# Optimization experiments

Hardware: AMD Instinct MI355X
Metric: run time of the kernel (lower is better)

Reference implementation:

```python
import jax, jax.numpy as jnp
import numpy as np

ACTION_NS = [3, 3, 2, 4, 24]        # forward_back, left_right, jump, sneak_sprint, attack_...
RANGE_STARTS = [6, 8, 10, 11, 14]   # action_ranges starts (indices 0..5 are commit + camera ops)
N_ACTIONS = 37
LOGIT_DIM = 36
MIN_DELTA = 0.5 / 2**3
MAX_STEP = 20
MAX_CAMSTEP = 6
B, NUM_INPUT, HIDDEN = 32768, 1024, 2048
D_IN = NUM_INPUT + 4 + LOGIT_DIM


def setup_inputs():
    key = jax.random.key(0)
    ks = jax.random.split(key, 12)
    inp = {
        "fc_input": jax.random.normal(ks[0], (B, NUM_INPUT), jnp.float32),
        "camera": jax.random.normal(ks[1], (B, 2), jnp.float32),
        "rand_u": jax.random.uniform(ks[2], (B,), jnp.float32),
        "W1": (jax.random.normal(ks[3], (D_IN, HIDDEN), jnp.float32) / np.sqrt(D_IN)).astype(jnp.float32),
        "b1": jnp.zeros((HIDDEN,), jnp.float32),
        "W2": (jax.random.normal(ks[4], (HIDDEN, N_ACTIONS), jnp.float32) / np.sqrt(HIDDEN)).astype(jnp.float32),
        "b2": jnp.zeros((N_ACTIONS,), jnp.float32),
    }
    names = ["act_fb", "act_lr", "act_jp", "act_ss", "act_atk"]
    for i, (nm, n) in enumerate(zip(names, ACTION_NS)):
        inp[nm] = jax.random.randint(ks[5 + i], (B,), 0, n, jnp.int32)
    return inp


def _discretize_scan(camera, acts):
    # Faithful jax version of the 20-step no_grad target/input construction loop.
    nB = camera.shape[0]
    cam0, cam1 = camera[:, 0], camera[:, 1]

    def step(carry, _):
        ac, delta, rdac, dch, cam_steps, committed, norm = carry
        oh = [jax.nn.one_hot(r, n, dtype=jnp.float32) for r, n in zip(rdac, ACTION_NS)]
        inp_vec = jnp.concatenate([ac] + oh + [delta[:, None], dch.astype(jnp.float32)[:, None]], axis=1)  # [B,40]
        norm = norm + (~committed).astype(jnp.float32)
        commit = ((jnp.abs(cam0) < 1e-5) & (jnp.abs(cam1) < 1e-5)) | (cam_steps >= MAX_CAMSTEP)
        for r, a in zip(rdac, acts):
            commit = commit & (r == a)
        dac = jnp.zeros((nB,), jnp.int32)
        modified = commit
        new_rdac = []
        for r, a, rs in zip(rdac, acts, RANGE_STARTS):
            disc = (~modified) & (r != a)
            dac = jnp.where(disc & (a == 0), r - 1 + rs, jnp.where(disc, a - 1 + rs, dac))
            new_rdac.append(jnp.where(disc, a, r))
            modified = modified | disc
        d2 = delta * 2.0
        # NOTE: original torch code compares cam[:,1] against ac[:,0]; bug preserved.
        dmask = (~modified) & (~dch) & ((jnp.abs(cam0 - ac[:, 0]) > d2) | (jnp.abs(cam1 - ac[:, 0]) > d2))
        dac = jnp.where(dmask, 5, dac)
        delta = jnp.where(dmask, jnp.clip(d2, -0.5, 0.5), delta)
        modified = modified | dmask
        sx = jnp.where(cam0 < ac[:, 0], -1.0, 1.0)
        sy = jnp.where(cam1 < ac[:, 1], -1.0, 1.0)
        quad = jnp.where(sx < 0, jnp.where(sy < 0, 1, 3), jnp.where(sy < 0, 2, 4)).astype(jnp.int32)
        dac = jnp.where(~modified, quad, dac)
        move = jnp.stack([sx, sy], axis=1) * delta[:, None]
        ac = jnp.where((~modified)[:, None], ac + move, ac)
        delta = jnp.where(~modified, delta * 0.5, delta)
        dch = dch | (~modified)
        cam_steps = cam_steps + (~modified).astype(jnp.int32)
        committed = committed | commit
        return (ac, delta, tuple(new_rdac), dch, cam_steps, committed, norm), (inp_vec, dac)

    init = (jnp.zeros((nB, 2), jnp.float32),
            jnp.full((nB,), MIN_DELTA, jnp.float32),
            tuple(jnp.zeros((nB,), jnp.int32) for _ in ACTION_NS),
            jnp.zeros((nB,), bool),
            jnp.zeros((nB,), jnp.int32),
            jnp.zeros((nB,), bool),
            jnp.zeros((nB,), jnp.float32))
    carry, (all_inputs, all_dacs) = jax.lax.scan(step, init, None, length=MAX_STEP)
    return all_inputs, all_dacs, carry[-1]  # [T,B,40], [T,B], norm [B]


def reference(fc_input, camera, rand_u, W1, b1, W2, b2, act_fb, act_lr, act_jp, act_ss, act_atk):
    acts = (act_fb, act_lr, act_jp, act_ss, act_atk)
    all_inputs, all_dacs, norm = _discretize_scan(camera, acts)
    rand_sam = jnp.minimum((rand_u * norm).astype(jnp.int32), MAX_STEP - 1)  # sample an uncommitted step
    idx = jnp.arange(fc_input.shape[0])
    sel = jax.lax.stop_gradient(all_inputs[rand_sam, idx])  # [B,40]
    tgt = jax.lax.stop_gradient(all_dacs[rand_sam, idx])    # [B]
    x = jnp.concatenate([fc_input, sel], axis=1)
    h = x @ W1 + b1
    h = h * jax.nn.sigmoid(h)  # swish
    logits = h @ W2 + b2
    logp = jax.nn.log_softmax(logits, axis=-1)
    loss = -jnp.take_along_axis(logp, tgt[:, None], axis=1)[:, 0]  # per-sample CE (reduction='none')
    return loss
```

## Files before the change

kernel.cpp:

```cpp
#include <hip/hip_runtime.h>
#include <hip/hip_bf16.h>
#include <stdint.h>

#define B_ROWS 32768
#define NUM_IN 1024
#define D_PAD2 1152
#define HID    2048
#define NPAD   64

typedef __attribute__((ext_vector_type(8))) short bf16x8;
typedef __attribute__((ext_vector_type(4))) float f32x4;
typedef unsigned short ushort_t;

__device__ __forceinline__ unsigned short f2bf(float f){
  union { float f; uint32_t u; } x; x.f = f;
  uint32_t u = x.u;
  return (unsigned short)((u + 0x7FFFu + ((u >> 16) & 1u)) >> 16);
}

__device__ __forceinline__ void gload16(const void* g, void* l){
  __builtin_amdgcn_global_load_lds((const __attribute__((address_space(1))) void*)g,
                                   (__attribute__((address_space(3))) void*)l, 16, 0, 0);
}

__device__ __forceinline__ int disc_step(
    float cam0, float cam1, const int a[5],
    float& ac0, float& ac1, float& delta,
    int r[5], bool& dch, int& cam_steps, bool& committed, float& norm)
{
  const int RS[5] = {6, 8, 10, 11, 14};
  norm += committed ? 0.0f : 1.0f;
  bool commit = ((fabsf(cam0) < 1e-5f) && (fabsf(cam1) < 1e-5f)) || (cam_steps >= 6);
  #pragma unroll
  for (int i = 0; i < 5; ++i) commit = commit && (r[i] == a[i]);
  int dac = 0;
  bool modified = commit;
  #pragma unroll
  for (int i = 0; i < 5; ++i){
    bool disc = (!modified) && (r[i] != a[i]);
    if (disc){
      dac = (a[i] == 0) ? (r[i] - 1 + RS[i]) : (a[i] - 1 + RS[i]);
      r[i] = a[i];
      modified = true;
    }
  }
  float d2 = delta * 2.0f;
  bool dmask = (!modified) && (!dch) &&
               ((fabsf(cam0 - ac0) > d2) || (fabsf(cam1 - ac0) > d2));
  if (dmask){ dac = 5; delta = fminf(d2, 0.5f); modified = true; }
  if (!modified){
    float sx = (cam0 < ac0) ? -1.0f : 1.0f;
    float sy = (cam1 < ac1) ? -1.0f : 1.0f;
    dac = (sx < 0.0f) ? ((sy < 0.0f) ? 1 : 3) : ((sy < 0.0f) ? 2 : 4);
    ac0 += sx * delta; ac1 += sy * delta;
    delta *= 0.5f;
    dch = true;
    cam_steps += 1;
  }
  committed = committed || commit;
  return dac;
}

__global__ void k_disc(const float* __restrict__ camera, const float* __restrict__ rand_u,
                       const int* __restrict__ afb, const int* __restrict__ alr,
                       const int* __restrict__ ajp, const int* __restrict__ ass,
                       const int* __restrict__ aat,
                       unsigned short* __restrict__ xb, int* __restrict__ tgt)
{
  int row = blockIdx.x * 256 + threadIdx.x;
  if (row >= B_ROWS) return;
  float cam0 = camera[2*row], cam1 = camera[2*row + 1];
  int a[5] = { afb[row], alr[row], ajp[row], ass[row], aat[row] };

  float ac0 = 0.f, ac1 = 0.f, delta = 0.0625f, norm = 0.f;
  int r[5] = {0,0,0,0,0};
  bool dch = false, committed = false; int cam_steps = 0;
  for (int t = 0; t < 20; ++t)
    disc_step(cam0, cam1, a, ac0, ac1, delta, r, dch, cam_steps, committed, norm);

  int rs = (int)(rand_u[row] * norm);
  if (rs > 19) rs = 19;
  if (rs < 0) rs = 0;

  ac0 = 0.f; ac1 = 0.f; delta = 0.0625f; norm = 0.f;
  r[0]=r[1]=r[2]=r[3]=r[4]=0; dch = false; committed = false; cam_steps = 0;
  for (int t = 0; t < rs; ++t)
    disc_step(cam0, cam1, a, ac0, ac1, delta, r, dch, cam_steps, committed, norm);

  float vec[40];
  #pragma unroll
  for (int j = 0; j < 40; ++j) vec[j] = 0.0f;
  vec[0] = ac0; vec[1] = ac1;
  const int offs[5] = {2, 5, 8, 10, 14};
  #pragma unroll
  for (int i = 0; i < 5; ++i) vec[offs[i] + r[i]] = 1.0f;
  vec[38] = delta; vec[39] = dch ? 1.0f : 0.0f;

  int dac = disc_step(cam0, cam1, a, ac0, ac1, delta, r, dch, cam_steps, committed, norm);
  tgt[row] = dac;

  unsigned short* o = xb + (size_t)row * D_PAD2 + NUM_IN;
  #pragma unroll
  for (int j = 0; j < 40; ++j) o[j] = f2bf(vec[j]);
  for (int j = 40; j < D_PAD2 - NUM_IN; ++j) o[j] = 0;
}

__global__ void k_fc(const float* __restrict__ fc, unsigned short* __restrict__ xb)
{
  int gid = blockIdx.x * 256 + threadIdx.x;
  int row = gid >> 7;
  int c   = gid & 127;
  const float4* p = (const float4*)(fc + (size_t)row * NUM_IN + c * 8);
  float4 f0 = p[0], f1 = p[1];
  unsigned short o[8] = { f2bf(f0.x), f2bf(f0.y), f2bf(f0.z), f2bf(f0.w),
                          f2bf(f1.x), f2bf(f1.y), f2bf(f1.z), f2bf(f1.w) };
  uint4 pk;
  pk.x = (uint32_t)o[0] | ((uint32_t)o[1] << 16);
  pk.y = (uint32_t)o[2] | ((uint32_t)o[3] << 16);
  pk.z = (uint32_t)o[4] | ((uint32_t)o[5] << 16);
  pk.w = (uint32_t)o[6] | ((uint32_t)o[7] << 16);
  *(uint4*)(xb + (size_t)row * D_PAD2 + c * 8) = pk;
}

__global__ void k_w1t(const float* __restrict__ W1, unsigned short* __restrict__ w1t)
{
  int idx = blockIdx.x * 256 + threadIdx.x;
  if (idx >= HID * D_PAD2) return;
  int n = idx / D_PAD2;
  int k = idx - n * D_PAD2;
  float v = (k < 1064) ? W1[(size_t)k * HID + n] : 0.0f;
  w1t[idx] = f2bf(v);
}

__global__ void k_w2t(const float* __restrict__ W2, unsigned short* __restrict__ w2t)
{
  int idx = blockIdx.x * 256 + threadIdx.x;
  if (idx >= NPAD * HID) return;
  int n = idx >> 11;
  int k = idx & (HID - 1);
  float v = (n < 37) ? W2[(size_t)k * 37 + n] : 0.0f;
  w2t[idx] = f2bf(v);
}

#define LDS_A0 0
#define LDS_A1 16384
#define LDS_B0 32768
#define LDS_B1 49152

#define STAGE(G, REG, ROW0, KT, HALF) do { \
    const ushort_t* s0_ = (G) + (size_t)((ROW0) + (HALF)*128 + srow) * D_PAD2 + ((KT) << 6) + scol; \
    gload16(s0_, lds + (REG) + (HALF)*8192 + t*8); \
    gload16(s0_ + (size_t)64 * D_PAD2, lds + (REG) + (HALF)*8192 + 4096 + t*8); \
  } while(0)

#define LDA_(REG, MH) do { \
    _Pragma("unroll") for (int mi_ = 0; mi_ < 4; ++mi_){ \
      const int row_ = arow_base + (MH)*64 + mi_*16; \
      _Pragma("unroll") for (int kk_ = 0; kk_ < 2; ++kk_) \
        aR[mi_][kk_] = *(const bf16x8*)(lds + (REG) + row_*64 + (((kk_*4+lg)^axor)<<3)); \
    } \
  } while(0)

#define LDB_(REG, NH, BR) do { \
    _Pragma("unroll") for (int ni_ = 0; ni_ < 2; ++ni_){ \
      const int row_ = brow_base + (NH)*32 + ni_*16; \
      _Pragma("unroll") for (int kk_ = 0; kk_ < 2; ++kk_) \
        BR[ni_][kk_] = *(const bf16x8*)(lds + (REG) + row_*64 + (((kk_*4+lg)^axor)<<3)); \
    } \
  } while(0)

#define MMA(MH, NH, BR) do { \
    __builtin_amdgcn_s_setprio(1); \
    _Pragma("unroll") for (int mi_ = 0; mi_ < 4; ++mi_) \
    _Pragma("unroll") for (int ni_ = 0; ni_ < 2; ++ni_) \
    _Pragma("unroll") for (int kk_ = 0; kk_ < 2; ++kk_) \
      acc[(MH)*4+mi_][(NH)*2+ni_] = __builtin_amdgcn_mfma_f32_16x16x32_bf16( \
          aR[mi_][kk_], BR[ni_][kk_], acc[(MH)*4+mi_][(NH)*2+ni_], 0, 0, 0); \
    __builtin_amdgcn_s_setprio(0); \
  } while(0)

#define BAR() __builtin_amdgcn_s_barrier()
#define WAIT_LGKM0() asm volatile("s_waitcnt lgkmcnt(0)" ::: "memory")
#define WAIT_VM6()   asm volatile("s_waitcnt vmcnt(6)" ::: "memory")
#define WAIT_VM0()   asm volatile("s_waitcnt vmcnt(0)" ::: "memory")

__global__ __launch_bounds__(512, 2) void k_gemm1(const ushort_t* __restrict__ xb,
                                                  const ushort_t* __restrict__ w1t,
                                                  const ushort_t* __restrict__ w2t,
                                                  const float* __restrict__ b1,
                                                  float* __restrict__ pbuf)
{
  __shared__ ushort_t lds[65536];
  const int t = threadIdx.x;
  const int lane = t & 63;
  const int wid = t >> 6, wm = wid >> 2, wn = wid & 3;
  const int lr = lane & 15, lg = lane >> 4;

  const int bid = blockIdx.x;
  const int swz = (bid & 7) * 128 + (bid >> 3);
  const int brow = (swz >> 3) << 8;
  const int bcol = (swz & 7) << 8;

  const int srow = t >> 3;
  const int scol = ((t & 7) ^ (srow & 7)) << 3;

  const int axor = lr & 7;
  const int arow_base = wm*128 + lr;
  const int brow_base = wn*64 + lr;

  f32x4 acc[8][4] = {};
  bf16x8 aR[4][2], bR0[2][2], bR1[2][2];

  STAGE(xb,  LDS_A0, brow, 0, 0);  STAGE(xb,  LDS_A0, brow, 0, 1);
  STAGE(w1t, LDS_B0, bcol, 0, 0);  STAGE(w1t, LDS_B0, bcol, 0, 1);
  STAGE(w1t, LDS_B1, bcol, 1, 0);  STAGE(w1t, LDS_B1, bcol, 1, 1);
  STAGE(xb,  LDS_A1, brow, 1, 0);
  WAIT_VM6();
  BAR();

  for (int i = 0; i < 9; ++i){
    const int c1 = 2*i + 1;
    const int n0 = (2*i + 2 <= 17) ? 2*i + 2 : 16;
    const int n1 = (2*i + 3 <= 17) ? 2*i + 3 : 17;

    LDA_(LDS_A0, 0); LDB_(LDS_B0, 0, bR0); LDB_(LDS_B0, 1, bR1);
    STAGE(xb, LDS_A1, brow, c1, 1);
    BAR(); WAIT_LGKM0();
    MMA(0, 0, bR0);
    BAR();
    STAGE(w1t, LDS_B0, bcol, n0, 0);
    BAR();
    MMA(0, 1, bR1);
    BAR();
    LDA_(LDS_A0, 1);
    STAGE(w1t, LDS_B0, bcol, n0, 1);
    BAR(); WAIT_LGKM0();
    MMA(1, 0, bR0);
    BAR();
    STAGE(xb, LDS_A0, brow, n0, 0);
    WAIT_VM6();
    BAR();
    MMA(1, 1, bR1);
    BAR();
    LDA_(LDS_A1, 0); LDB_(LDS_B1, 0, bR0); LDB_(LDS_B1, 1, bR1);
    STAGE(xb, LDS_A0, brow, n0, 1);
    BAR(); WAIT_LGKM0();
    MMA(0, 0, bR0);
    BAR();
    STAGE(w1t, LDS_B1, bcol, n1, 0);
    BAR();
    MMA(0, 1, bR1);
    BAR();
    LDA_(LDS_A1, 1);
    STAGE(w1t, LDS_B1, bcol, n1, 1);
    BAR(); WAIT_LGKM0();
    MMA(1, 0, bR0);
    BAR();
    STAGE(xb, LDS_A1, brow, n1, 0);
    WAIT_VM6();
    BAR();
    MMA(1, 1, bR1);
    BAR();
  }

  WAIT_VM0();
  BAR();

  float b1v[4];
  #pragma unroll
  for (int ni = 0; ni < 4; ++ni) b1v[ni] = b1[bcol + wn*64 + ni*16 + lr];

  #pragma unroll
  for (int mi = 0; mi < 8; ++mi){
    #pragma unroll
    for (int ni = 0; ni < 4; ++ni){
      const int col = wn*64 + ni*16 + lr;
      #pragma unroll
      for (int i2 = 0; i2 < 4; ++i2){
        const int row = wm*128 + mi*16 + lg*4 + i2;
        float v = acc[mi][ni][i2] + b1v[ni];
        float s = v / (1.0f + __expf(-v));
        const int chunk = (col >> 3) ^ (row & 7);
        lds[row*256 + chunk*8 + (col & 7)] = f2bf(s);
      }
    }
  }
  __syncthreads();

  const int rb = wid * 32;
  f32x4 acc2[2][4] = {};
  #pragma unroll
  for (int ks = 0; ks < 8; ++ks){
    bf16x8 a2[2], b2f[4];
    #pragma unroll
    for (int m = 0; m < 2; ++m){
      const int row = rb + m*16 + lr;
      a2[m] = *(const bf16x8*)(lds + row*256 + (((ks*4+lg) ^ (lr & 7)) << 3));
    }
    #pragma unroll
    for (int ni = 0; ni < 4; ++ni)
      b2f[ni] = *(const bf16x8*)(w2t + (size_t)(ni*16 + lr) * HID + bcol + ks*32 + lg*8);
    #pragma unroll
    for (int m = 0; m < 2; ++m)
      #pragma unroll
      for (int ni = 0; ni < 4; ++ni)
        acc2[m][ni] = __builtin_amdgcn_mfma_f32_16x16x32_bf16(a2[m], b2f[ni], acc2[m][ni], 0, 0, 0);
  }

  const int cb = bcol >> 8;
  #pragma unroll
  for (int m = 0; m < 2; ++m)
    #pragma unroll
    for (int ni = 0; ni < 4; ++ni)
      #pragma unroll
      for (int i2 = 0; i2 < 4; ++i2){
        const int r = brow + rb + m*16 + lg*4 + i2;
        pbuf[((size_t)cb << 21) + ((size_t)r << 6) + ni*16 + lr] = acc2[m][ni][i2];
      }
}

__global__ __launch_bounds__(256) void k_red(const float* __restrict__ pbuf,
                                             const float* __restrict__ b2,
                                             const int* __restrict__ tgt,
                                             float* __restrict__ loss)
{
  const int lane = threadIdx.x & 63, w = threadIdx.x >> 6;
  const int row0 = blockIdx.x * 128 + w * 32;
  const float bias = (lane < 37) ? b2[lane] : 0.0f;
  for (int i = 0; i < 32; ++i){
    const int r = row0 + i;
    float s = 0.0f;
    #pragma unroll
    for (int cb = 0; cb < 8; ++cb)
      s += pbuf[((size_t)cb << 21) + ((size_t)r << 6) + lane];
    float x = (lane < 37) ? (s + bias) : -1e30f;
    float m = x;
    #pragma unroll
    for (int off = 1; off < 64; off <<= 1) m = fmaxf(m, __shfl_xor(m, off, 64));
    float e = __expf(x - m);
    float se = e;
    #pragma unroll
    for (int off = 1; off < 64; off <<= 1) se += __shfl_xor(se, off, 64);
    const int tg = tgt[r];
    const float pick = __shfl(x, tg, 64);
    if (lane == 0) loss[r] = m + __logf(se) - pick;
  }
}

extern "C" void kernel_launch(void* const* d_in, const int* in_sizes, int n_in,
                              void* d_out, int out_size, void* d_ws, size_t ws_size,
                              hipStream_t stream)
{
  (void)in_sizes; (void)n_in; (void)out_size; (void)ws_size;
  const float* fc  = (const float*)d_in[0];
  const float* cam = (const float*)d_in[1];
  const float* ru  = (const float*)d_in[2];
  const float* W1  = (const float*)d_in[3];
  const float* b1  = (const float*)d_in[4];
  const float* W2  = (const float*)d_in[5];
  const float* b2  = (const float*)d_in[6];
  const int* afb = (const int*)d_in[7];
  const int* alr = (const int*)d_in[8];
  const int* ajp = (const int*)d_in[9];
  const int* ass = (const int*)d_in[10];
  const int* aat = (const int*)d_in[11];
  float* loss = (float*)d_out;

  char* ws = (char*)d_ws;
  unsigned short* xb  = (unsigned short*)(ws);
  unsigned short* w1t = (unsigned short*)(ws + 75497472);
  unsigned short* w2t = (unsigned short*)(ws + 80216064);
  int*            tgt = (int*)           (ws + 80478208);
  float*          pbuf= (float*)         (ws + 80609280);

  k_fc  <<<16384, 256, 0, stream>>>(fc, xb);
  k_w1t <<<(HID * D_PAD2 + 255) / 256, 256, 0, stream>>>(W1, w1t);
  k_w2t <<<(NPAD * HID + 255) / 256, 256, 0, stream>>>(W2, w2t);
  k_disc<<<(B_ROWS + 255) / 256, 256, 0, stream>>>(cam, ru, afb, alr, ajp, ass, aat, xb, tgt);

  k_gemm1<<<(B_ROWS/256) * (HID/256), 512, 0, stream>>>(xb, w1t, w2t, b1, pbuf);
  k_red  <<<B_ROWS / 128, 256, 0, stream>>>(pbuf, b2, tgt, loss);
}
```

Baseline: 284.1 us.

## Fuse prep kernels, shrink K padding to 1088, prefetch W2 fragments

Merges the four preprocessing kernels (fc conversion, W1/W2 transposes, discretization) into one launch with block-range dispatch. K padding shrinks from 1152 to 1088, so the GEMM main loop drops one K-tile pair and gets an explicit epilogue for the last tile. W2 fragments are loaded into registers early, before the swish epilogue, to hide global latency in the second GEMM. These cut launch overhead and GEMM work, at the cost of more register pressure from the 32 prefetched bf16x8 fragments.

```diff
diff --git a/kernel.cpp b/kernel.cpp
--- a/kernel.cpp
+++ b/kernel.cpp
@@ -4,7 +4,7 @@
 
 #define B_ROWS 32768
 #define NUM_IN 1024
-#define D_PAD2 1152
+#define D_PAD2 1088
 #define HID    2048
 #define NPAD   64
 
@@ -61,14 +61,48 @@
   return dac;
 }
 
-__global__ void k_disc(const float* __restrict__ camera, const float* __restrict__ rand_u,
+__global__ void k_prep(const float* __restrict__ fc, const float* __restrict__ W1,
+                       const float* __restrict__ W2,
+                       const float* __restrict__ camera, const float* __restrict__ rand_u,
                        const int* __restrict__ afb, const int* __restrict__ alr,
                        const int* __restrict__ ajp, const int* __restrict__ ass,
                        const int* __restrict__ aat,
-                       unsigned short* __restrict__ xb, int* __restrict__ tgt)
-{
-  int row = blockIdx.x * 256 + threadIdx.x;
-  if (row >= B_ROWS) return;
+                       unsigned short* __restrict__ xb, unsigned short* __restrict__ w1t,
+                       unsigned short* __restrict__ w2t, int* __restrict__ tgt)
+{
+  const int b = blockIdx.x;
+  const int tid = threadIdx.x;
+  if (b < 16384){
+    int gid = b * 256 + tid;
+    int row = gid >> 7;
+    int c   = gid & 127;
+    const float4* p = (const float4*)(fc + (size_t)row * NUM_IN + c * 8);
+    float4 f0 = p[0], f1 = p[1];
+    uint4 pk;
+    pk.x = (uint32_t)f2bf(f0.x) | ((uint32_t)f2bf(f0.y) << 16);
+    pk.y = (uint32_t)f2bf(f0.z) | ((uint32_t)f2bf(f0.w) << 16);
+    pk.z = (uint32_t)f2bf(f1.x) | ((uint32_t)f2bf(f1.y) << 16);
+    pk.w = (uint32_t)f2bf(f1.z) | ((uint32_t)f2bf(f1.w) << 16);
+    *(uint4*)(xb + (size_t)row * D_PAD2 + c * 8) = pk;
+    return;
+  }
+  if (b < 25088){
+    int idx = (b - 16384) * 256 + tid;
+    int n = idx / D_PAD2;
+    int k = idx - n * D_PAD2;
+    float v = (k < 1064) ? W1[(size_t)k * HID + n] : 0.0f;
+    w1t[idx] = f2bf(v);
+    return;
+  }
+  if (b < 25600){
+    int idx = (b - 25088) * 256 + tid;
+    int n = idx >> 11;
+    int k = idx & (HID - 1);
+    float v = (n < 37) ? W2[(size_t)k * 37 + n] : 0.0f;
+    w2t[idx] = f2bf(v);
+    return;
+  }
+  int row = (b - 25600) * 256 + tid;
   float cam0 = camera[2*row], cam1 = camera[2*row + 1];
   int a[5] = { afb[row], alr[row], ajp[row], ass[row], aat[row] };
 
@@ -102,44 +136,8 @@
   unsigned short* o = xb + (size_t)row * D_PAD2 + NUM_IN;
   #pragma unroll
   for (int j = 0; j < 40; ++j) o[j] = f2bf(vec[j]);
-  for (int j = 40; j < D_PAD2 - NUM_IN; ++j) o[j] = 0;
-}
-
-__global__ void k_fc(const float* __restrict__ fc, unsigned short* __restrict__ xb)
-{
-  int gid = blockIdx.x * 256 + threadIdx.x;
-  int row = gid >> 7;
-  int c   = gid & 127;
-  const float4* p = (const float4*)(fc + (size_t)row * NUM_IN + c * 8);
-  float4 f0 = p[0], f1 = p[1];
-  unsigned short o[8] = { f2bf(f0.x), f2bf(f0.y), f2bf(f0.z), f2bf(f0.w),
-                          f2bf(f1.x), f2bf(f1.y), f2bf(f1.z), f2bf(f1.w) };
-  uint4 pk;
-  pk.x = (uint32_t)o[0] | ((uint32_t)o[1] << 16);
-  pk.y = (uint32_t)o[2] | ((uint32_t)o[3] << 16);
-  pk.z = (uint32_t)o[4] | ((uint32_t)o[5] << 16);
-  pk.w = (uint32_t)o[6] | ((uint32_t)o[7] << 16);
-  *(uint4*)(xb + (size_t)row * D_PAD2 + c * 8) = pk;
-}
-
-__global__ void k_w1t(const float* __restrict__ W1, unsigned short* __restrict__ w1t)
-{
-  int idx = blockIdx.x * 256 + threadIdx.x;
-  if (idx >= HID * D_PAD2) return;
-  int n = idx / D_PAD2;
-  int k = idx - n * D_PAD2;
-  float v = (k < 1064) ? W1[(size_t)k * HID + n] : 0.0f;
-  w1t[idx] = f2bf(v);
-}
-
-__global__ void k_w2t(const float* __restrict__ W2, unsigned short* __restrict__ w2t)
-{
-  int idx = blockIdx.x * 256 + threadIdx.x;
-  if (idx >= NPAD * HID) return;
-  int n = idx >> 11;
-  int k = idx & (HID - 1);
-  float v = (n < 37) ? W2[(size_t)k * 37 + n] : 0.0f;
-  w2t[idx] = f2bf(v);
+  #pragma unroll
+  for (int j = 40; j < 64; ++j) o[j] = 0;
 }
 
 #define LDS_A0 0
@@ -218,10 +216,10 @@
   WAIT_VM6();
   BAR();
 
-  for (int i = 0; i < 9; ++i){
+  for (int i = 0; i < 8; ++i){
     const int c1 = 2*i + 1;
-    const int n0 = (2*i + 2 <= 17) ? 2*i + 2 : 16;
-    const int n1 = (2*i + 3 <= 17) ? 2*i + 3 : 17;
+    const int n0 = 2*i + 2;
+    const int n1 = (2*i + 3 <= 16) ? 2*i + 3 : 16;
 
     LDA_(LDS_A0, 0); LDB_(LDS_B0, 0, bR0); LDB_(LDS_B0, 1, bR1);
     STAGE(xb, LDS_A1, brow, c1, 1);
@@ -262,6 +260,18 @@
     MMA(1, 1, bR1);
     BAR();
   }
+
+  LDA_(LDS_A0, 0); LDB_(LDS_B0, 0, bR0); LDB_(LDS_B0, 1, bR1);
+  MMA(0, 0, bR0); MMA(0, 1, bR1);
+  LDA_(LDS_A0, 1);
+  MMA(1, 0, bR0); MMA(1, 1, bR1);
+
+  bf16x8 w2fA[4][4];
+  #pragma unroll
+  for (int ks = 0; ks < 4; ++ks)
+    #pragma unroll
+    for (int ni = 0; ni < 4; ++ni)
+      w2fA[ks][ni] = *(const bf16x8*)(w2t + (size_t)(ni*16 + lr) * HID + bcol + ks*32 + lg*8);
 
   WAIT_VM0();
   BAR();
@@ -287,24 +297,29 @@
   }
   __syncthreads();
 
+  bf16x8 w2fB[4][4];
+  #pragma unroll
+  for (int ks = 0; ks < 4; ++ks)
+    #pragma unroll
+    for (int ni = 0; ni < 4; ++ni)
+      w2fB[ks][ni] = *(const bf16x8*)(w2t + (size_t)(ni*16 + lr) * HID + bcol + (ks+4)*32 + lg*8);
+
   const int rb = wid * 32;
   f32x4 acc2[2][4] = {};
   #pragma unroll
   for (int ks = 0; ks < 8; ++ks){
-    bf16x8 a2[2], b2f[4];
+    bf16x8 a2[2];
     #pragma unroll
     for (int m = 0; m < 2; ++m){
       const int row = rb + m*16 + lr;
       a2[m] = *(const bf16x8*)(lds + row*256 + (((ks*4+lg) ^ (lr & 7)) << 3));
     }
     #pragma unroll
-    for (int ni = 0; ni < 4; ++ni)
-      b2f[ni] = *(const bf16x8*)(w2t + (size_t)(ni*16 + lr) * HID + bcol + ks*32 + lg*8);
-    #pragma unroll
     for (int m = 0; m < 2; ++m)
       #pragma unroll
       for (int ni = 0; ni < 4; ++ni)
-        acc2[m][ni] = __builtin_amdgcn_mfma_f32_16x16x32_bf16(a2[m], b2f[ni], acc2[m][ni], 0, 0, 0);
+        acc2[m][ni] = __builtin_amdgcn_mfma_f32_16x16x32_bf16(
+            a2[m], (ks < 4) ? w2fA[ks & 3][ni] : w2fB[ks & 3][ni], acc2[m][ni], 0, 0, 0);
   }
 
   const int cb = bcol >> 8;
@@ -368,16 +383,13 @@
 
   char* ws = (char*)d_ws;
   unsigned short* xb  = (unsigned short*)(ws);
-  unsigned short* w1t = (unsigned short*)(ws + 75497472);
-  unsigned short* w2t = (unsigned short*)(ws + 80216064);
-  int*            tgt = (int*)           (ws + 80478208);
-  float*          pbuf= (float*)         (ws + 80609280);
-
-  k_fc  <<<16384, 256, 0, stream>>>(fc, xb);
-  k_w1t <<<(HID * D_PAD2 + 255) / 256, 256, 0, stream>>>(W1, w1t);
-  k_w2t <<<(NPAD * HID + 255) / 256, 256, 0, stream>>>(W2, w2t);
-  k_disc<<<(B_ROWS + 255) / 256, 256, 0, stream>>>(cam, ru, afb, alr, ajp, ass, aat, xb, tgt);
-
+  unsigned short* w1t = (unsigned short*)(ws + 71303168);
+  unsigned short* w2t = (unsigned short*)(ws + 75759616);
+  int*            tgt = (int*)           (ws + 76021760);
+  float*          pbuf= (float*)         (ws + 76152832);
+
+  k_prep<<<25728, 256, 0, stream>>>(fc, W1, W2, cam, ru, afb, alr, ajp, ass, aat,
+                                    xb, w1t, w2t, tgt);
   k_gemm1<<<(B_ROWS/256) * (HID/256), 512, 0, stream>>>(xb, w1t, w2t, b1, pbuf);
   k_red  <<<B_ROWS / 128, 256, 0, stream>>>(pbuf, b2, tgt, loss);
 }
```

New measurement: 275.6 us. 1.03x faster.
